# Optimization experiments

Measured on AMD Instinct MI355X. Metric: run time of the kernel, lower is better.

Reference implementation:

```python
import jax, jax.numpy as jnp
import numpy as np

THRESHOLD = 0.9  # module buffer _threshold (starting_threshold)


def setup_inputs() -> dict:
    key = jax.random.key(0)
    k_x, k_w = jax.random.split(key)
    B, T, D = 64, 577, 768
    x = jax.random.normal(k_x, (B, T, D), dtype=jnp.float32)
    # nn.Linear(in_dim, 1): weight [1, D] -> stored as vector [D], bias [1]
    w = jax.random.normal(k_w, (D,), dtype=jnp.float32) * (1.0 / np.sqrt(D))
    b = jnp.zeros((1,), dtype=jnp.float32)
    return {"x": x, "w": w, "b": b}


def reference(x, w, b):
    B, T, D = x.shape
    density = int(T * THRESHOLD)  # static: int(577*0.9) = 519
    # head: Linear(D,1) -> sigmoid -> [B, T]  (dropout is identity in eval)
    prob = jax.nn.sigmoid(jnp.einsum('btd,d->bt', x, w) + b[0])
    # keep top-`density` tokens by score (sorted descending, like torch.topk)
    _, top_idx = jax.lax.top_k(prob, density)
    tokens = jnp.take_along_axis(x, top_idx[..., None], axis=1)  # [B, density, D]
    # bottom (T - density) tokens: topk(largest=False) == topk of -prob,
    # which yields values sorted ascending in prob, matching torch
    n_skip = T - density  # 58 > 0
    neg_vals, skip_idx = jax.lax.top_k(-prob, n_skip)
    skip_tokens = jnp.take_along_axis(x, skip_idx[..., None], axis=1)  # [B, n_skip, D]
    weights = jax.nn.softmax(-neg_vals, axis=-1)  # softmax over skipped probs
    summary_token = jnp.sum(skip_tokens * weights[..., None], axis=1, keepdims=True)  # [B,1,D]
    return tokens, skip_tokens, summary_token
```

## Files before the change

### kernel.cpp

```cpp
#include <hip/hip_runtime.h>
#include <math.h>

#define BB 64
#define TT 577
#define DD 768
#define DENS 519
#define NSKIP 58
#define NROWS (BB * TT)

typedef float vf4 __attribute__((ext_vector_type(4)));

__device__ inline unsigned long long key_of(double z) {
    long long b = __double_as_longlong(z);
    return (b < 0) ? ~(unsigned long long)b
                   : ((unsigned long long)b | 0x8000000000000000ULL);
}
__device__ inline double key_inv(unsigned long long k) {
    long long b = (k >> 63) ? (long long)(k & 0x7fffffffffffffffULL)
                            : ~(long long)k;
    return __longlong_as_double(b);
}

__global__ __launch_bounds__(256) void k_prob(const float* __restrict__ x,
                                              const float* __restrict__ w,
                                              const float* __restrict__ bias,
                                              unsigned long long* __restrict__ keys) {
    int wave = (int)((blockIdx.x * blockDim.x + threadIdx.x) >> 6);
    int lane = threadIdx.x & 63;
    if (wave >= NROWS) return;
    const float4* r4 = (const float4*)(x + (size_t)wave * DD);
    const float4* w4 = (const float4*)w;
    double acc = 0.0;
#pragma unroll
    for (int i = 0; i < 3; ++i) {
        float4 a = r4[lane + 64 * i];
        float4 b = w4[lane + 64 * i];
        acc += (double)a.x * (double)b.x + (double)a.y * (double)b.y
             + (double)a.z * (double)b.z + (double)a.w * (double)b.w;
    }
#pragma unroll
    for (int off = 32; off; off >>= 1)
        acc += __shfl_down(acc, off, 64);
    if (lane == 0) {
        keys[wave] = key_of(acc + (double)bias[0]);
    }
}

__global__ __launch_bounds__(256) void k_rank(const unsigned long long* __restrict__ keys,
                                              int* __restrict__ tok_src,
                                              int* __restrict__ skip_src,
                                              unsigned long long* __restrict__ skip_key) {
    int wave = (int)((blockIdx.x * blockDim.x + threadIdx.x) >> 6);
    int lane = threadIdx.x & 63;
    if (wave >= NROWS) return;
    int b = wave / TT;
    int i = wave - b * TT;
    const unsigned long long* kb = keys + b * TT;
    unsigned long long ki = kb[i];
    int rd = 0, ra = 0;
#pragma unroll
    for (int c = 0; c < 10; ++c) {
        int j = lane + 64 * c;
        if (j < TT) {
            unsigned long long kj = kb[j];
            bool tie = (kj == ki) & (j < i);
            rd += ((kj > ki) | tie) ? 1 : 0;
            ra += ((kj < ki) | tie) ? 1 : 0;
        }
    }
    unsigned long long pack = ((unsigned long long)(unsigned)rd << 32) | (unsigned)ra;
#pragma unroll
    for (int off = 32; off; off >>= 1)
        pack += __shfl_down(pack, off, 64);
    if (lane == 0) {
        int r_desc = (int)(pack >> 32);
        int r_asc  = (int)(pack & 0xffffffffu);
        if (r_desc < DENS) {
            tok_src[b * DENS + r_desc] = i;
        } else {
            skip_src[b * NSKIP + r_asc] = i;
            skip_key[b * NSKIP + r_asc] = ki;
        }
    }
}

__global__ __launch_bounds__(768) void k_soft(const float* __restrict__ x,
                                              const int* __restrict__ skip_src,
                                              const unsigned long long* __restrict__ skip_key,
                                              float* __restrict__ summary) {
    __shared__ float wsh[NSKIP];
    __shared__ int   ssh[NSKIP];
    int b = blockIdx.x;
    int t = threadIdx.x;
    if (t < NSKIP) ssh[t] = skip_src[b * NSKIP + t];
    if (t < 64) {
        double pv = -1.0e300;
        if (t < NSKIP) {
            double z = key_inv(skip_key[b * NSKIP + t]);
            pv = 1.0 / (1.0 + exp(-z));
        }
        double m = pv;
#pragma unroll
        for (int off = 32; off; off >>= 1) {
            double o = __shfl_down(m, off, 64);
            m = (o > m) ? o : m;
        }
        m = __shfl(m, 0, 64);
        double e = (t < NSKIP) ? exp(pv - m) : 0.0;
        double s = e;
#pragma unroll
        for (int off = 32; off; off >>= 1)
            s += __shfl_down(s, off, 64);
        s = __shfl(s, 0, 64);
        if (t < NSKIP) wsh[t] = (float)(e / s);
    }
    __syncthreads();
    float acc = 0.f;
    const float* xb = x + (size_t)b * TT * DD;
    for (int k = 0; k < NSKIP; ++k)
        acc += wsh[k] * xb[(size_t)ssh[k] * DD + t];
    summary[(size_t)b * DD + t] = acc;
}

__global__ __launch_bounds__(256) void k_gather(const float* __restrict__ x,
                                                const int* __restrict__ tok_src,
                                                const int* __restrict__ skip_src,
                                                float* __restrict__ out) {
    int wave = (int)((blockIdx.x * blockDim.x + threadIdx.x) >> 6);
    int lane = threadIdx.x & 63;
    if (wave >= NROWS) return;
    int b = wave / TT;
    int k = wave - b * TT;
    int src;
    size_t dst;
    if (k < DENS) {
        src = tok_src[b * DENS + k];
        dst = (size_t)(b * DENS + k) * DD;
    } else {
        int k2 = k - DENS;
        src = skip_src[b * NSKIP + k2];
        dst = (size_t)BB * DENS * DD + (size_t)(b * NSKIP + k2) * DD;
    }
    const vf4* s4 = (const vf4*)(x + ((size_t)b * TT + src) * DD);
    vf4* d4 = (vf4*)(out + dst);
#pragma unroll
    for (int i = 0; i < 3; ++i) {
        vf4 v = s4[lane + 64 * i];
        __builtin_nontemporal_store(v, &d4[lane + 64 * i]);
    }
}

extern "C" void kernel_launch(void* const* d_in, const int* in_sizes, int n_in,
                              void* d_out, int out_size, void* d_ws, size_t ws_size,
                              hipStream_t stream) {
    const float* x    = (const float*)d_in[0];
    const float* w    = (const float*)d_in[1];
    const float* bias = (const float*)d_in[2];
    float* out = (float*)d_out;
    char* ws = (char*)d_ws;

    unsigned long long* keys = (unsigned long long*)ws;
    int* tok_src  = (int*)(ws + 295424);
    int* skip_src = (int*)(ws + 295424 + 132864);
    unsigned long long* skip_key =
        (unsigned long long*)(ws + 295424 + 132864 + 14848);

    const int nblk = NROWS / 4;

    k_prob<<<nblk, 256, 0, stream>>>(x, w, bias, keys);
    k_rank<<<nblk, 256, 0, stream>>>(keys, tok_src, skip_src, skip_key);
    k_soft<<<BB, 768, 0, stream>>>(x, skip_src, skip_key,
                                   out + (size_t)BB * (DENS + NSKIP) * DD);
    k_gather<<<nblk, 256, 0, stream>>>(x, tok_src, skip_src, out);
}
```

Baseline: 241.1 us.

## Fuse rank and gather into a scatter kernel writing rows by computed rank

```diff
diff --git a/kernel.cpp b/kernel.cpp
--- a/kernel.cpp
+++ b/kernel.cpp
@@ -46,10 +46,11 @@
     }
 }
 
-__global__ __launch_bounds__(256) void k_rank(const unsigned long long* __restrict__ keys,
-                                              int* __restrict__ tok_src,
-                                              int* __restrict__ skip_src,
-                                              unsigned long long* __restrict__ skip_key) {
+__global__ __launch_bounds__(256) void k_rankscatter(const float* __restrict__ x,
+                                                     const unsigned long long* __restrict__ keys,
+                                                     int* __restrict__ skip_src,
+                                                     unsigned long long* __restrict__ skip_key,
+                                                     float* __restrict__ out) {
     int wave = (int)((blockIdx.x * blockDim.x + threadIdx.x) >> 6);
     int lane = threadIdx.x & 63;
     if (wave >= NROWS) return;
@@ -71,16 +72,26 @@
     unsigned long long pack = ((unsigned long long)(unsigned)rd << 32) | (unsigned)ra;
 #pragma unroll
     for (int off = 32; off; off >>= 1)
-        pack += __shfl_down(pack, off, 64);
-    if (lane == 0) {
-        int r_desc = (int)(pack >> 32);
-        int r_asc  = (int)(pack & 0xffffffffu);
-        if (r_desc < DENS) {
-            tok_src[b * DENS + r_desc] = i;
-        } else {
+        pack += __shfl_xor(pack, off, 64);
+    int r_desc = (int)(pack >> 32);
+    int r_asc  = (int)(pack & 0xffffffffu);
+
+    size_t dst;
+    if (r_desc < DENS) {
+        dst = (size_t)(b * DENS + r_desc) * DD;
+    } else {
+        dst = (size_t)BB * DENS * DD + (size_t)(b * NSKIP + r_asc) * DD;
+        if (lane == 0) {
             skip_src[b * NSKIP + r_asc] = i;
             skip_key[b * NSKIP + r_asc] = ki;
         }
+    }
+    const vf4* s4 = (const vf4*)(x + ((size_t)b * TT + i) * DD);
+    vf4* d4 = (vf4*)(out + dst);
+#pragma unroll
+    for (int c = 0; c < 3; ++c) {
+        vf4 v = s4[lane + 64 * c];
+        __builtin_nontemporal_store(v, &d4[lane + 64 * c]);
     }
 }
 
@@ -122,34 +133,6 @@
     summary[(size_t)b * DD + t] = acc;
 }
 
-__global__ __launch_bounds__(256) void k_gather(const float* __restrict__ x,
-                                                const int* __restrict__ tok_src,
-                                                const int* __restrict__ skip_src,
-                                                float* __restrict__ out) {
-    int wave = (int)((blockIdx.x * blockDim.x + threadIdx.x) >> 6);
-    int lane = threadIdx.x & 63;
-    if (wave >= NROWS) return;
-    int b = wave / TT;
-    int k = wave - b * TT;
-    int src;
-    size_t dst;
-    if (k < DENS) {
-        src = tok_src[b * DENS + k];
-        dst = (size_t)(b * DENS + k) * DD;
-    } else {
-        int k2 = k - DENS;
-        src = skip_src[b * NSKIP + k2];
-        dst = (size_t)BB * DENS * DD + (size_t)(b * NSKIP + k2) * DD;
-    }
-    const vf4* s4 = (const vf4*)(x + ((size_t)b * TT + src) * DD);
-    vf4* d4 = (vf4*)(out + dst);
-#pragma unroll
-    for (int i = 0; i < 3; ++i) {
-        vf4 v = s4[lane + 64 * i];
-        __builtin_nontemporal_store(v, &d4[lane + 64 * i]);
-    }
-}
-
 extern "C" void kernel_launch(void* const* d_in, const int* in_sizes, int n_in,
                               void* d_out, int out_size, void* d_ws, size_t ws_size,
                               hipStream_t stream) {
@@ -160,16 +143,14 @@
     char* ws = (char*)d_ws;
 
     unsigned long long* keys = (unsigned long long*)ws;
-    int* tok_src  = (int*)(ws + 295424);
-    int* skip_src = (int*)(ws + 295424 + 132864);
+    int* skip_src = (int*)(ws + 295424);
     unsigned long long* skip_key =
-        (unsigned long long*)(ws + 295424 + 132864 + 14848);
+        (unsigned long long*)(ws + 295424 + 14848);
 
     const int nblk = NROWS / 4;
 
     k_prob<<<nblk, 256, 0, stream>>>(x, w, bias, keys);
-    k_rank<<<nblk, 256, 0, stream>>>(keys, tok_src, skip_src, skip_key);
+    k_rankscatter<<<nblk, 256, 0, stream>>>(x, keys, skip_src, skip_key, out);
     k_soft<<<BB, 768, 0, stream>>>(x, skip_src, skip_key,
                                    out + (size_t)BB * (DENS + NSKIP) * DD);
-    k_gather<<<nblk, 256, 0, stream>>>(x, tok_src, skip_src, out);
 }
```

Result: faster. 223.4 us (-7.3%).
